# Kernel optimization log

Hardware: AMD Instinct MI355X
Metric: run time of the kernel (lower is better)

The kernel has to match this reference:

```python
import jax, jax.numpy as jnp
import numpy as np

GUIDING_LAMBDA = 0.6
N_EXPERT = 4


def setup_inputs() -> dict:
    key = jax.random.key(0)
    ks = jax.random.split(key, 8)
    B, L, H, E = 8, 128, 768, 7
    D = 2 * (H + E + 1)  # 1552 pair-embedding dim
    s = 0.02
    return {
        "utter_repr": jax.random.normal(ks[0], (B, L, H), jnp.float32),
        "speaker_ids": jax.random.randint(ks[1], (B, L), 0, 2),
        "emo_W": jax.random.normal(ks[2], (H, E), jnp.float32) * s,
        "emo_b": jnp.zeros((E,), jnp.float32),
        "gate_W": jax.random.normal(ks[3], (D, N_EXPERT), jnp.float32) * s,
        "gate_b": jnp.zeros((N_EXPERT,), jnp.float32),
        "exp_W1": jax.random.normal(ks[4], (N_EXPERT, D, 256), jnp.float32) * s,
        "exp_b1": jnp.zeros((N_EXPERT, 256), jnp.float32),
        "exp_W2": jax.random.normal(ks[5], (N_EXPERT, 256, 2), jnp.float32) * s,
        "exp_b2": jnp.zeros((N_EXPERT, 2), jnp.float32),
    }


def reference(utter_repr, speaker_ids, emo_W, emo_b, gate_W, gate_b,
              exp_W1, exp_b1, exp_W2, exp_b2):
    B, L, H = utter_repr.shape
    flat = utter_repr.reshape(B * L, H)
    # emotion classification head (dropout = identity in eval)
    emotion_pred = flat @ emo_W + emo_b                      # [B*L, 7]
    spk = speaker_ids.reshape(B * L, 1).astype(flat.dtype)
    concat = jnp.concatenate([flat, emotion_pred, spk], axis=-1)
    concat = concat.reshape(B, L, -1)                        # [B, L, 776]
    # all (t, end_t) pairs with t <= end_t  (vectorized form of the nested loops)
    end_idx, t_idx = np.tril_indices(L)                      # P = L(L+1)/2
    pair = jnp.concatenate([concat[:, t_idx], concat[:, end_idx]], axis=-1)
    pair_flat = pair.reshape(-1, pair.shape[-1])             # [B*P, 1552]
    # gating on detached pair embedding
    gating = jax.nn.softmax(
        jax.lax.stop_gradient(pair_flat) @ gate_W + gate_b, axis=-1)
    # mechanical subtask label (speaker / emotion agreement -> 4-way one-hot)
    s_eq = speaker_ids[:, t_idx] == speaker_ids[:, end_idx]  # [B, P]
    emo = jnp.argmax(emotion_pred.reshape(B, L, -1), axis=-1)
    e_eq = emo[:, t_idx] == emo[:, end_idx]
    lbl = jnp.where(s_eq & e_eq, 0,
                    jnp.where(s_eq, 1, jnp.where(e_eq, 2, 3)))
    label = jax.nn.one_hot(lbl.reshape(-1), N_EXPERT, dtype=pair_flat.dtype)
    gating = GUIDING_LAMBDA * label + (1.0 - GUIDING_LAMBDA) * gating
    # experts: Linear(1552,256) -> Linear(256,2), no activation between
    hidden = jnp.einsum('pd,edh->eph', pair_flat, exp_W1) + exp_b1[:, None, :]
    expert_out = jnp.einsum('eph,ehc->epc', hidden, exp_W2) + exp_b2[:, None, :]
    cause_pred = jnp.einsum('pe,epc->pc', gating, expert_out)  # [B*P, 2]
    return emotion_pred, cause_pred
```

## Files before the change

kernel.cpp:

```cpp
#include <hip/hip_runtime.h>
#include <math.h>

#define B_   8
#define L_   128
#define H_   768
#define E_   7
#define NE_  4
#define HALF_ 776
#define D_   1552
#define PPB_ 8256
#define NROW_ 1024
#define EMO_OUT_ 7168

#define WEFF_OFF 0
#define BEFF_OFF 12416
#define EARG_OFF 12424
#define GLO_OFF  13448
#define GHI_OFF  17544
#define AA_OFF   21640
#define BB_OFF   29832

#define WEFF_BLOCKS 97

__global__ __launch_bounds__(256)
void k_weff(const float* __restrict__ w1,
            const float* __restrict__ w2,
            const float* __restrict__ b1,
            const float* __restrict__ b2,
            float* __restrict__ ws) {
    int blk = blockIdx.x;
    if (blk < WEFF_BLOCKS) {
        __shared__ float red[4][64][2];
        int dl = threadIdx.x & 63;
        int hc = threadIdx.x >> 6;
        int idx = blk * 64 + dl;
        int e = idx / D_, d = idx % D_;
        const float* w1row = w1 + ((size_t)e * D_ + d) * 256 + hc * 64;
        const float* w2e   = w2 + e * 512 + hc * 128;
        float a0 = 0.f, a1 = 0.f;
        #pragma unroll
        for (int h = 0; h < 64; h += 4) {
            float4 wv = *(const float4*)(w1row + h);
            float4 p0 = *(const float4*)(w2e + 2 * h);
            float4 p1 = *(const float4*)(w2e + 2 * h + 4);
            a0 += wv.x * p0.x + wv.y * p0.z + wv.z * p1.x + wv.w * p1.z;
            a1 += wv.x * p0.y + wv.y * p0.w + wv.z * p1.y + wv.w * p1.w;
        }
        red[hc][dl][0] = a0;
        red[hc][dl][1] = a1;
        __syncthreads();
        if (hc == 0) {
            float s0 = red[0][dl][0] + red[1][dl][0] + red[2][dl][0] + red[3][dl][0];
            float s1 = red[0][dl][1] + red[1][dl][1] + red[2][dl][1] + red[3][dl][1];
            ws[WEFF_OFF + d * 8 + e * 2 + 0] = s0;
            ws[WEFF_OFF + d * 8 + e * 2 + 1] = s1;
        }
    } else {
        int lane = threadIdx.x;
        if (lane < 64) {
            int j = lane >> 3;
            int part = lane & 7;
            int e = j >> 1, c = j & 1;
            const float* w2e = w2 + e * 512;
            const float* b1e = b1 + e * 256;
            float acc = 0.f;
            #pragma unroll 8
            for (int h = part * 32; h < part * 32 + 32; ++h)
                acc += b1e[h] * w2e[2 * h + c];
            acc += __shfl_down(acc, 4, 64);
            acc += __shfl_down(acc, 2, 64);
            acc += __shfl_down(acc, 1, 64);
            if (part == 0) ws[BEFF_OFF + j] = acc + b2[j];
        }
    }
}

__global__ __launch_bounds__(64)
void k_row(const float* __restrict__ utter,
           const int*   __restrict__ spk,
           const float* __restrict__ emoW,
           const float* __restrict__ emoB,
           const float* __restrict__ gateW,
           float* __restrict__ ws,
           float* __restrict__ out) {
    int row  = blockIdx.x;
    int lane = threadIdx.x;
    const float* x = utter + (size_t)row * H_;

    float aemo[E_];
    float ag[24];
    #pragma unroll
    for (int j = 0; j < E_; ++j) aemo[j] = 0.f;
    #pragma unroll
    for (int k = 0; k < 24; ++k) ag[k] = 0.f;

    #pragma unroll
    for (int i = 0; i < 3; ++i) {
        int d = i * 256 + lane * 4;
        float4 xv = *(const float4*)(x + d);
        float xr[4] = {xv.x, xv.y, xv.z, xv.w};

        float ewf[28];
        const float* ew = emoW + d * E_;
        #pragma unroll
        for (int q = 0; q < 7; ++q) {
            float4 t = *(const float4*)(ew + q * 4);
            ewf[q * 4 + 0] = t.x; ewf[q * 4 + 1] = t.y;
            ewf[q * 4 + 2] = t.z; ewf[q * 4 + 3] = t.w;
        }
        #pragma unroll
        for (int r = 0; r < 4; ++r)
            #pragma unroll
            for (int j = 0; j < E_; ++j) aemo[j] += xr[r] * ewf[r * 7 + j];

        float gl[16], gh[16];
        const float* glp = gateW + d * NE_;
        const float* ghp = gateW + (HALF_ + d) * NE_;
        #pragma unroll
        for (int q = 0; q < 4; ++q) {
            float4 t0 = *(const float4*)(glp + q * 4);
            gl[q * 4 + 0] = t0.x; gl[q * 4 + 1] = t0.y;
            gl[q * 4 + 2] = t0.z; gl[q * 4 + 3] = t0.w;
            float4 t1 = *(const float4*)(ghp + q * 4);
            gh[q * 4 + 0] = t1.x; gh[q * 4 + 1] = t1.y;
            gh[q * 4 + 2] = t1.z; gh[q * 4 + 3] = t1.w;
        }
        #pragma unroll
        for (int r = 0; r < 4; ++r)
            #pragma unroll
            for (int k = 0; k < NE_; ++k) {
                ag[k]     += xr[r] * gl[r * 4 + k];
                ag[4 + k] += xr[r] * gh[r * 4 + k];
            }

        float wl[32], wh[32];
        const float* wlp = ws + WEFF_OFF + d * 8;
        const float* whp = ws + WEFF_OFF + (HALF_ + d) * 8;
        #pragma unroll
        for (int q = 0; q < 8; ++q) {
            float4 t0 = *(const float4*)(wlp + q * 4);
            wl[q * 4 + 0] = t0.x; wl[q * 4 + 1] = t0.y;
            wl[q * 4 + 2] = t0.z; wl[q * 4 + 3] = t0.w;
            float4 t1 = *(const float4*)(whp + q * 4);
            wh[q * 4 + 0] = t1.x; wh[q * 4 + 1] = t1.y;
            wh[q * 4 + 2] = t1.z; wh[q * 4 + 3] = t1.w;
        }
        #pragma unroll
        for (int r = 0; r < 4; ++r)
            #pragma unroll
            for (int k = 0; k < 8; ++k) {
                ag[8 + k]  += xr[r] * wl[r * 8 + k];
                ag[16 + k] += xr[r] * wh[r * 8 + k];
            }
    }

    #pragma unroll
    for (int j = 0; j < E_; ++j) {
        float v = aemo[j];
        for (int o = 32; o > 0; o >>= 1) v += __shfl_xor(v, o, 64);
        aemo[j] = v + emoB[j];
    }

    if (lane == 0) {
        int best = 0; float bv = aemo[0];
        #pragma unroll
        for (int j = 1; j < E_; ++j) if (aemo[j] > bv) { bv = aemo[j]; best = j; }
        ((int*)ws)[EARG_OFF + row] = best;
        #pragma unroll
        for (int j = 0; j < E_; ++j) out[row * E_ + j] = aemo[j];
    }

    if (lane < 8) {
        float v = (lane < E_) ? aemo[lane] : (float)spk[row];
        int d = H_ + lane;
        const float* glp = gateW + d * NE_;
        const float* ghp = gateW + (HALF_ + d) * NE_;
        #pragma unroll
        for (int k = 0; k < NE_; ++k) { ag[k] += v * glp[k]; ag[4 + k] += v * ghp[k]; }
        const float* wlp = ws + WEFF_OFF + d * 8;
        const float* whp = ws + WEFF_OFF + (HALF_ + d) * 8;
        #pragma unroll
        for (int k = 0; k < 8; ++k) { ag[8 + k] += v * wlp[k]; ag[16 + k] += v * whp[k]; }
    }

    #pragma unroll
    for (int k = 0; k < 24; ++k) {
        float v = ag[k];
        for (int o = 32; o > 0; o >>= 1) v += __shfl_xor(v, o, 64);
        ag[k] = v;
    }

    if (lane == 0) {
        #pragma unroll
        for (int k = 0; k < NE_; ++k) {
            ws[GLO_OFF + row * 4 + k] = ag[k];
            ws[GHI_OFF + row * 4 + k] = ag[4 + k];
        }
        #pragma unroll
        for (int k = 0; k < 8; ++k) {
            ws[AA_OFF + row * 8 + k] = ag[8 + k];
            ws[BB_OFF + row * 8 + k] = ag[16 + k];
        }
    }
}

__global__ __launch_bounds__(128)
void k_pair(const int* __restrict__ spk,
            const float* __restrict__ ws,
            const float* __restrict__ gate_b,
            float* __restrict__ out) {
    int b   = blockIdx.x >> 7;
    int end = blockIdx.x & 127;
    int t   = threadIdx.x;
    if (t > end) return;

    int rt = b * L_ + t;
    int re = b * L_ + end;

    float gb[4] = {gate_b[0], gate_b[1], gate_b[2], gate_b[3]};
    float be[8];
    {
        float4 b0 = *(const float4*)(ws + BEFF_OFF);
        float4 b1v = *(const float4*)(ws + BEFF_OFF + 4);
        be[0]=b0.x; be[1]=b0.y; be[2]=b0.z; be[3]=b0.w;
        be[4]=b1v.x; be[5]=b1v.y; be[6]=b1v.z; be[7]=b1v.w;
    }

    float4 glo = *(const float4*)(ws + GLO_OFF + rt * 4);
    float4 ghi = *(const float4*)(ws + GHI_OFF + re * 4);
    float lg[NE_] = {glo.x + ghi.x + gb[0], glo.y + ghi.y + gb[1],
                     glo.z + ghi.z + gb[2], glo.w + ghi.w + gb[3]};

    float m = fmaxf(fmaxf(lg[0], lg[1]), fmaxf(lg[2], lg[3]));
    float ex[NE_], s = 0.f;
    #pragma unroll
    for (int k = 0; k < NE_; ++k) { ex[k] = expf(lg[k] - m); s += ex[k]; }
    float inv = 0.4f / s;

    const int* earg = (const int*)ws + EARG_OFF;
    bool seq = (spk[rt] == spk[re]);
    bool eeq = (earg[rt] == earg[re]);
    int lbl = (seq && eeq) ? 0 : (seq ? 1 : (eeq ? 2 : 3));

    float A[8], Bv[8];
    {
        float4 a0 = *(const float4*)(ws + AA_OFF + rt * 8);
        float4 a1 = *(const float4*)(ws + AA_OFF + rt * 8 + 4);
        A[0]=a0.x; A[1]=a0.y; A[2]=a0.z; A[3]=a0.w;
        A[4]=a1.x; A[5]=a1.y; A[6]=a1.z; A[7]=a1.w;
        float4 v0 = *(const float4*)(ws + BB_OFF + re * 8);
        float4 v1 = *(const float4*)(ws + BB_OFF + re * 8 + 4);
        Bv[0]=v0.x; Bv[1]=v0.y; Bv[2]=v0.z; Bv[3]=v0.w;
        Bv[4]=v1.x; Bv[5]=v1.y; Bv[6]=v1.z; Bv[7]=v1.w;
    }

    float o0 = 0.f, o1 = 0.f;
    #pragma unroll
    for (int e = 0; e < NE_; ++e) {
        float g = ex[e] * inv + ((e == lbl) ? 0.6f : 0.f);
        o0 += g * (A[e * 2 + 0] + Bv[e * 2 + 0] + be[e * 2 + 0]);
        o1 += g * (A[e * 2 + 1] + Bv[e * 2 + 1] + be[e * 2 + 1]);
    }

    int p = ((end * (end + 1)) >> 1) + t;
    float* cp = out + EMO_OUT_ + ((size_t)b * PPB_ + p) * 2;
    cp[0] = o0;
    cp[1] = o1;
}

extern "C" void kernel_launch(void* const* d_in, const int* in_sizes, int n_in,
                              void* d_out, int out_size, void* d_ws, size_t ws_size,
                              hipStream_t stream) {
    const float* utter = (const float*)d_in[0];
    const int*   spk   = (const int*)  d_in[1];
    const float* emoW  = (const float*)d_in[2];
    const float* emoB  = (const float*)d_in[3];
    const float* gateW = (const float*)d_in[4];
    const float* gateB = (const float*)d_in[5];
    const float* w1    = (const float*)d_in[6];
    const float* b1    = (const float*)d_in[7];
    const float* w2    = (const float*)d_in[8];
    const float* b2    = (const float*)d_in[9];

    float* ws  = (float*)d_ws;
    float* out = (float*)d_out;

    k_weff<<<WEFF_BLOCKS + 1, 256, 0, stream>>>(w1, w2, b1, b2, ws);
    k_row<<<NROW_, 64, 0, stream>>>(utter, spk, emoW, emoB, gateW, ws, out);
    k_pair<<<B_ * L_, 128, 0, stream>>>(spk, ws, gateB, out);
}
```

Baseline: 95.30 us.

## Rebalance parallelism across weff, row and pair kernels

Three parallelisation changes at once. k_weff gets twice as many blocks, each covering half the hidden chunk with an 8-way shared reduction. k_row uses three wavefronts per row, one per 256-wide slice of H, combining their partial sums through shared memory. k_pair switches from a triangular per-end grid, where many threads exit early, to a dense flat grid over all pairs, recovering (end, t) with a sqrt-based inverse. The aim is higher occupancy and less idle work, at the cost of an extra shared-memory sync and some index arithmetic.

```diff
diff --git a/kernel.cpp b/kernel.cpp
--- a/kernel.cpp
+++ b/kernel.cpp
@@ -20,7 +20,7 @@
 #define AA_OFF   21640
 #define BB_OFF   29832
 
-#define WEFF_BLOCKS 97
+#define WEFF_BLOCKS 194
 
 __global__ __launch_bounds__(256)
 void k_weff(const float* __restrict__ w1,
@@ -30,16 +30,16 @@
             float* __restrict__ ws) {
     int blk = blockIdx.x;
     if (blk < WEFF_BLOCKS) {
-        __shared__ float red[4][64][2];
-        int dl = threadIdx.x & 63;
-        int hc = threadIdx.x >> 6;
-        int idx = blk * 64 + dl;
+        __shared__ float red[8][32][2];
+        int dl = threadIdx.x & 31;
+        int hc = threadIdx.x >> 5;
+        int idx = blk * 32 + dl;
         int e = idx / D_, d = idx % D_;
-        const float* w1row = w1 + ((size_t)e * D_ + d) * 256 + hc * 64;
-        const float* w2e   = w2 + e * 512 + hc * 128;
+        const float* w1row = w1 + ((size_t)e * D_ + d) * 256 + hc * 32;
+        const float* w2e   = w2 + e * 512 + hc * 64;
         float a0 = 0.f, a1 = 0.f;
         #pragma unroll
-        for (int h = 0; h < 64; h += 4) {
+        for (int h = 0; h < 32; h += 4) {
             float4 wv = *(const float4*)(w1row + h);
             float4 p0 = *(const float4*)(w2e + 2 * h);
             float4 p1 = *(const float4*)(w2e + 2 * h + 4);
@@ -50,8 +50,9 @@
         red[hc][dl][1] = a1;
         __syncthreads();
         if (hc == 0) {
-            float s0 = red[0][dl][0] + red[1][dl][0] + red[2][dl][0] + red[3][dl][0];
-            float s1 = red[0][dl][1] + red[1][dl][1] + red[2][dl][1] + red[3][dl][1];
+            float s0 = 0.f, s1 = 0.f;
+            #pragma unroll
+            for (int q = 0; q < 8; ++q) { s0 += red[q][dl][0]; s1 += red[q][dl][1]; }
             ws[WEFF_OFF + d * 8 + e * 2 + 0] = s0;
             ws[WEFF_OFF + d * 8 + e * 2 + 1] = s1;
         }
@@ -75,7 +76,7 @@
     }
 }
 
-__global__ __launch_bounds__(64)
+__global__ __launch_bounds__(192)
 void k_row(const float* __restrict__ utter,
            const int*   __restrict__ spk,
            const float* __restrict__ emoW,
@@ -84,7 +85,8 @@
            float* __restrict__ ws,
            float* __restrict__ out) {
     int row  = blockIdx.x;
-    int lane = threadIdx.x;
+    int wv   = threadIdx.x >> 6;
+    int lane = threadIdx.x & 63;
     const float* x = utter + (size_t)row * H_;
 
     float aemo[E_];
@@ -94,95 +96,69 @@
     #pragma unroll
     for (int k = 0; k < 24; ++k) ag[k] = 0.f;
 
-    #pragma unroll
-    for (int i = 0; i < 3; ++i) {
-        int d = i * 256 + lane * 4;
-        float4 xv = *(const float4*)(x + d);
-        float xr[4] = {xv.x, xv.y, xv.z, xv.w};
-
-        float ewf[28];
-        const float* ew = emoW + d * E_;
-        #pragma unroll
-        for (int q = 0; q < 7; ++q) {
-            float4 t = *(const float4*)(ew + q * 4);
-            ewf[q * 4 + 0] = t.x; ewf[q * 4 + 1] = t.y;
-            ewf[q * 4 + 2] = t.z; ewf[q * 4 + 3] = t.w;
-        }
-        #pragma unroll
-        for (int r = 0; r < 4; ++r)
-            #pragma unroll
-            for (int j = 0; j < E_; ++j) aemo[j] += xr[r] * ewf[r * 7 + j];
-
-        float gl[16], gh[16];
-        const float* glp = gateW + d * NE_;
-        const float* ghp = gateW + (HALF_ + d) * NE_;
-        #pragma unroll
-        for (int q = 0; q < 4; ++q) {
-            float4 t0 = *(const float4*)(glp + q * 4);
-            gl[q * 4 + 0] = t0.x; gl[q * 4 + 1] = t0.y;
-            gl[q * 4 + 2] = t0.z; gl[q * 4 + 3] = t0.w;
-            float4 t1 = *(const float4*)(ghp + q * 4);
-            gh[q * 4 + 0] = t1.x; gh[q * 4 + 1] = t1.y;
-            gh[q * 4 + 2] = t1.z; gh[q * 4 + 3] = t1.w;
-        }
-        #pragma unroll
-        for (int r = 0; r < 4; ++r)
-            #pragma unroll
-            for (int k = 0; k < NE_; ++k) {
-                ag[k]     += xr[r] * gl[r * 4 + k];
-                ag[4 + k] += xr[r] * gh[r * 4 + k];
-            }
-
-        float wl[32], wh[32];
-        const float* wlp = ws + WEFF_OFF + d * 8;
-        const float* whp = ws + WEFF_OFF + (HALF_ + d) * 8;
-        #pragma unroll
-        for (int q = 0; q < 8; ++q) {
-            float4 t0 = *(const float4*)(wlp + q * 4);
-            wl[q * 4 + 0] = t0.x; wl[q * 4 + 1] = t0.y;
-            wl[q * 4 + 2] = t0.z; wl[q * 4 + 3] = t0.w;
-            float4 t1 = *(const float4*)(whp + q * 4);
-            wh[q * 4 + 0] = t1.x; wh[q * 4 + 1] = t1.y;
-            wh[q * 4 + 2] = t1.z; wh[q * 4 + 3] = t1.w;
-        }
-        #pragma unroll
-        for (int r = 0; r < 4; ++r)
-            #pragma unroll
-            for (int k = 0; k < 8; ++k) {
-                ag[8 + k]  += xr[r] * wl[r * 8 + k];
-                ag[16 + k] += xr[r] * wh[r * 8 + k];
-            }
-    }
+    int d = wv * 256 + lane * 4;
+    float4 xv = *(const float4*)(x + d);
+    float xr[4] = {xv.x, xv.y, xv.z, xv.w};
+
+    float ewf[28];
+    const float* ew = emoW + d * E_;
+    #pragma unroll
+    for (int q = 0; q < 7; ++q) {
+        float4 t = *(const float4*)(ew + q * 4);
+        ewf[q * 4 + 0] = t.x; ewf[q * 4 + 1] = t.y;
+        ewf[q * 4 + 2] = t.z; ewf[q * 4 + 3] = t.w;
+    }
+    #pragma unroll
+    for (int r = 0; r < 4; ++r)
+        #pragma unroll
+        for (int j = 0; j < E_; ++j) aemo[j] += xr[r] * ewf[r * 7 + j];
+
+    float gl[16], gh[16];
+    const float* glp = gateW + d * NE_;
+    const float* ghp = gateW + (HALF_ + d) * NE_;
+    #pragma unroll
+    for (int q = 0; q < 4; ++q) {
+        float4 t0 = *(const float4*)(glp + q * 4);
+        gl[q * 4 + 0] = t0.x; gl[q * 4 + 1] = t0.y;
+        gl[q * 4 + 2] = t0.z; gl[q * 4 + 3] = t0.w;
+        float4 t1 = *(const float4*)(ghp + q * 4);
+        gh[q * 4 + 0] = t1.x; gh[q * 4 + 1] = t1.y;
+        gh[q * 4 + 2] = t1.z; gh[q * 4 + 3] = t1.w;
+    }
+    #pragma unroll
+    for (int r = 0; r < 4; ++r)
+        #pragma unroll
+        for (int k = 0; k < NE_; ++k) {
+            ag[k]     += xr[r] * gl[r * 4 + k];
+            ag[4 + k] += xr[r] * gh[r * 4 + k];
+        }
+
+    float wl[32], wh[32];
+    const float* wlp = ws + WEFF_OFF + d * 8;
+    const float* whp = ws + WEFF_OFF + (HALF_ + d) * 8;
+    #pragma unroll
+    for (int q = 0; q < 8; ++q) {
+        float4 t0 = *(const float4*)(wlp + q * 4);
+        wl[q * 4 + 0] = t0.x; wl[q * 4 + 1] = t0.y;
+        wl[q * 4 + 2] = t0.z; wl[q * 4 + 3] = t0.w;
+        float4 t1 = *(const float4*)(whp + q * 4);
+        wh[q * 4 + 0] = t1.x; wh[q * 4 + 1] = t1.y;
+        wh[q * 4 + 2] = t1.z; wh[q * 4 + 3] = t1.w;
+    }
+    #pragma unroll
+    for (int r = 0; r < 4; ++r)
+        #pragma unroll
+        for (int k = 0; k < 8; ++k) {
+            ag[8 + k]  += xr[r] * wl[r * 8 + k];
+            ag[16 + k] += xr[r] * wh[r * 8 + k];
+        }
 
     #pragma unroll
     for (int j = 0; j < E_; ++j) {
         float v = aemo[j];
         for (int o = 32; o > 0; o >>= 1) v += __shfl_xor(v, o, 64);
-        aemo[j] = v + emoB[j];
-    }
-
-    if (lane == 0) {
-        int best = 0; float bv = aemo[0];
-        #pragma unroll
-        for (int j = 1; j < E_; ++j) if (aemo[j] > bv) { bv = aemo[j]; best = j; }
-        ((int*)ws)[EARG_OFF + row] = best;
-        #pragma unroll
-        for (int j = 0; j < E_; ++j) out[row * E_ + j] = aemo[j];
-    }
-
-    if (lane < 8) {
-        float v = (lane < E_) ? aemo[lane] : (float)spk[row];
-        int d = H_ + lane;
-        const float* glp = gateW + d * NE_;
-        const float* ghp = gateW + (HALF_ + d) * NE_;
-        #pragma unroll
-        for (int k = 0; k < NE_; ++k) { ag[k] += v * glp[k]; ag[4 + k] += v * ghp[k]; }
-        const float* wlp = ws + WEFF_OFF + d * 8;
-        const float* whp = ws + WEFF_OFF + (HALF_ + d) * 8;
-        #pragma unroll
-        for (int k = 0; k < 8; ++k) { ag[8 + k] += v * wlp[k]; ag[16 + k] += v * whp[k]; }
-    }
-
+        aemo[j] = v;
+    }
     #pragma unroll
     for (int k = 0; k < 24; ++k) {
         float v = ag[k];
@@ -190,32 +166,86 @@
         ag[k] = v;
     }
 
+    __shared__ float red[3][31];
     if (lane == 0) {
         #pragma unroll
-        for (int k = 0; k < NE_; ++k) {
-            ws[GLO_OFF + row * 4 + k] = ag[k];
-            ws[GHI_OFF + row * 4 + k] = ag[4 + k];
-        }
-        #pragma unroll
-        for (int k = 0; k < 8; ++k) {
-            ws[AA_OFF + row * 8 + k] = ag[8 + k];
-            ws[BB_OFF + row * 8 + k] = ag[16 + k];
+        for (int j = 0; j < E_; ++j) red[wv][j] = aemo[j];
+        #pragma unroll
+        for (int k = 0; k < 24; ++k) red[wv][E_ + k] = ag[k];
+    }
+    __syncthreads();
+
+    if (wv == 0) {
+        float tot[31];
+        #pragma unroll
+        for (int k = 0; k < 31; ++k) tot[k] = red[0][k] + red[1][k] + red[2][k];
+        float aem[E_];
+        #pragma unroll
+        for (int j = 0; j < E_; ++j) aem[j] = tot[j] + emoB[j];
+
+        if (lane == 0) {
+            int best = 0; float bv = aem[0];
+            #pragma unroll
+            for (int j = 1; j < E_; ++j) if (aem[j] > bv) { bv = aem[j]; best = j; }
+            ((int*)ws)[EARG_OFF + row] = best;
+            #pragma unroll
+            for (int j = 0; j < E_; ++j) out[row * E_ + j] = aem[j];
+        }
+
+        float tail[24];
+        #pragma unroll
+        for (int k = 0; k < 24; ++k) tail[k] = 0.f;
+        if (lane < 8) {
+            float v = (lane < E_) ? aem[lane] : (float)spk[row];
+            int dd = H_ + lane;
+            const float* tgl = gateW + dd * NE_;
+            const float* tgh = gateW + (HALF_ + dd) * NE_;
+            #pragma unroll
+            for (int k = 0; k < NE_; ++k) { tail[k] = v * tgl[k]; tail[4 + k] = v * tgh[k]; }
+            const float* twl = ws + WEFF_OFF + dd * 8;
+            const float* twh = ws + WEFF_OFF + (HALF_ + dd) * 8;
+            #pragma unroll
+            for (int k = 0; k < 8; ++k) { tail[8 + k] = v * twl[k]; tail[16 + k] = v * twh[k]; }
+            #pragma unroll
+            for (int k = 0; k < 24; ++k) {
+                float t = tail[k];
+                t += __shfl_xor(t, 4, 8);
+                t += __shfl_xor(t, 2, 8);
+                t += __shfl_xor(t, 1, 8);
+                tail[k] = t;
+            }
+        }
+
+        if (lane == 0) {
+            #pragma unroll
+            for (int k = 0; k < NE_; ++k) {
+                ws[GLO_OFF + row * 4 + k] = tot[E_ + k] + tail[k];
+                ws[GHI_OFF + row * 4 + k] = tot[E_ + 4 + k] + tail[4 + k];
+            }
+            #pragma unroll
+            for (int k = 0; k < 8; ++k) {
+                ws[AA_OFF + row * 8 + k] = tot[E_ + 8 + k] + tail[8 + k];
+                ws[BB_OFF + row * 8 + k] = tot[E_ + 16 + k] + tail[16 + k];
+            }
         }
     }
 }
 
-__global__ __launch_bounds__(128)
+__global__ __launch_bounds__(256)
 void k_pair(const int* __restrict__ spk,
             const float* __restrict__ ws,
             const float* __restrict__ gate_b,
             float* __restrict__ out) {
-    int b   = blockIdx.x >> 7;
-    int end = blockIdx.x & 127;
-    int t   = threadIdx.x;
-    if (t > end) return;
+    int tid = blockIdx.x * 256 + threadIdx.x;
+    int b = tid / PPB_;
+    int p = tid - b * PPB_;
+    int e = (int)((sqrtf(8.f * (float)p + 1.f) - 1.f) * 0.5f);
+    while ((e + 1) * (e + 2) / 2 <= p) ++e;
+    while (e * (e + 1) / 2 > p) --e;
+    int t = p - e * (e + 1) / 2;
 
     int rt = b * L_ + t;
-    int re = b * L_ + end;
+    int re = b * L_ + e;
 
     float gb[4] = {gate_b[0], gate_b[1], gate_b[2], gate_b[3]};
     float be[8];
@@ -256,13 +286,12 @@
 
     float o0 = 0.f, o1 = 0.f;
     #pragma unroll
-    for (int e = 0; e < NE_; ++e) {
-        float g = ex[e] * inv + ((e == lbl) ? 0.6f : 0.f);
-        o0 += g * (A[e * 2 + 0] + Bv[e * 2 + 0] + be[e * 2 + 0]);
-        o1 += g * (A[e * 2 + 1] + Bv[e * 2 + 1] + be[e * 2 + 1]);
-    }
-
-    int p = ((end * (end + 1)) >> 1) + t;
+    for (int ee = 0; ee < NE_; ++ee) {
+        float g = ex[ee] * inv + ((ee == lbl) ? 0.6f : 0.f);
+        o0 += g * (A[ee * 2 + 0] + Bv[ee * 2 + 0] + be[ee * 2 + 0]);
+        o1 += g * (A[ee * 2 + 1] + Bv[ee * 2 + 1] + be[ee * 2 + 1]);
+    }
+
     float* cp = out + EMO_OUT_ + ((size_t)b * PPB_ + p) * 2;
     cp[0] = o0;
     cp[1] = o1;
@@ -286,6 +315,6 @@
     float* out = (float*)d_out;
 
     k_weff<<<WEFF_BLOCKS + 1, 256, 0, stream>>>(w1, w2, b1, b2, ws);
-    k_row<<<NROW_, 64, 0, stream>>>(utter, spk, emoW, emoB, gateW, ws, out);
-    k_pair<<<B_ * L_, 128, 0, stream>>>(spk, ws, gateB, out);
+    k_row<<<NROW_, 192, 0, stream>>>(utter, spk, emoW, emoB, gateW, ws, out);
+    k_pair<<<258, 256, 0, stream>>>(spk, ws, gateB, out);
 }
```

New measurement: 92.73 us. 1.03x faster.
